# Performance work log

Measured on AMD Instinct MI355X. Metric: run time of the kernel, lower is better.

The kernel has to match this reference:

```python
import jax, jax.numpy as jnp
import numpy as np

EPS = 1e-5
C_M, C, C_Z = 256, 32, 128
N_SEQ, N_RES = 256, 1024


def setup_inputs() -> dict:
    key = jax.random.key(0)
    k1, k2, k3 = jax.random.split(key, 3)
    msa = jax.random.normal(k1, (N_SEQ, N_RES, C_M), dtype=jnp.float32)
    norm_w = jnp.ones((C_M,), dtype=jnp.float32)
    norm_b = jnp.zeros((C_M,), dtype=jnp.float32)
    w_ab = jax.random.normal(k2, (C, C_M), dtype=jnp.float32) * (1.0 / np.sqrt(C_M))
    b_ab = jnp.zeros((C,), dtype=jnp.float32)
    w_out = jax.random.normal(k3, (C_Z, C * C), dtype=jnp.float32) * (1.0 / C)
    b_out = jnp.zeros((C_Z,), dtype=jnp.float32)
    return {"msa": msa, "norm_w": norm_w, "norm_b": norm_b,
            "w_ab": w_ab, "b_ab": b_ab, "w_out": w_out, "b_out": b_out}


def reference(msa, norm_w, norm_b, w_ab, b_ab, w_out, b_out):
    # msa: (s, r, c_m) -> (r, s, c_m)
    x = jnp.transpose(msa, (1, 0, 2))
    s = x.shape[1]
    # LayerNorm over c_m
    mu = jnp.mean(x, axis=-1, keepdims=True)
    var = jnp.mean(jnp.square(x - mu), axis=-1, keepdims=True)
    xn = (x - mu) * jax.lax.rsqrt(var + EPS) * norm_w + norm_b
    # a == b: same linear applied twice to same input in the original
    a = jnp.einsum('rsm,cm->rsc', xn, w_ab) + b_ab          # (r, s, c)
    # mean over s of outer product == batched A^T A / s  -> (r, c, c)
    o = jnp.einsum('rsx,rsy->rxy', a, a) / s
    o = o.reshape(o.shape[0], C * C)                        # (r, c*c)
    pre_pair = jnp.einsum('rk,zk->rz', o, w_out) + b_out    # (r, c_z)
    r = pre_pair.shape[0]
    # unsqueeze(1).expand(r, r, c_z)
    pair = jnp.broadcast_to(pre_pair[:, None, :], (r, r, C_Z))
    return pair
```

## Files before the change

### kernel.cpp

```cpp
#include <hip/hip_runtime.h>

#define NSEQ 256
#define NRES 1024
#define CM   256
#define CC   32
#define CZ   128
#define EPS  1e-5f
#define SROW (NRES * CM)
#define MCH  16
#define XPAD 20

typedef float f4v __attribute__((ext_vector_type(4)));

__global__ void opm_setup(const float* __restrict__ nw,
                          const float* __restrict__ nb,
                          const float* __restrict__ w_ab,
                          const float* __restrict__ b_ab,
                          float* __restrict__ wt_g,
                          float* __restrict__ k12)
{
    __shared__ float wls[CM * CC];
    const int t = threadIdx.x;
    const float nwm = nw[t];
    #pragma unroll
    for (int c = 0; c < CC; ++c)
        wls[t * CC + c] = nwm * w_ab[c * CM + t];
    __syncthreads();
    for (int i = t; i < CM * CC; i += 256) wt_g[i] = wls[i];
    if (t < CC) {
        float k1 = 0.f, k2 = 0.f;
        for (int m = 0; m < CM; ++m) {
            k1 += wls[m * CC + t];
            k2 = fmaf(nb[m], w_ab[t * CM + m], k2);
        }
        k12[t]      = k1;
        k12[CC + t] = k2 + b_ab[t];
    }
}

__launch_bounds__(256, 3)
__global__ void opm_compute(const float* __restrict__ msa,
                            const float* __restrict__ wt_g,
                            const float* __restrict__ k12,
                            const float* __restrict__ w_out,
                            const float* __restrict__ b_out,
                            float* __restrict__ pre_out)
{
    __shared__ float wt[CM * CC];
    __shared__ float xt[NSEQ * XPAD];

    const int tid  = threadIdx.x;
    const int r    = blockIdx.x;
    const int wave = tid >> 6;

    const int sc4 = tid & 3;
    const int sg4 = tid >> 2;
    const int sc8 = tid & 7;
    const int sg8 = tid >> 3;
    const int c0  = sc8 << 2;

    const float* xr = msa + (size_t)r * CM;

    float4 pf[4];
    #pragma unroll
    for (int k = 0; k < 4; ++k)
        pf[k] = *(const float4*)(xr + (size_t)(sg4 + (k << 6)) * SROW + (sc4 << 2));

    #pragma unroll
    for (int k = 0; k < 8; ++k) {
        const int i = (tid + (k << 8)) << 2;
        *(float4*)&wt[i] = *(const float4*)&wt_g[i];
    }

    float G[8][4];
    #pragma unroll
    for (int j = 0; j < 8; ++j) {
        G[j][0] = 0.f; G[j][1] = 0.f; G[j][2] = 0.f; G[j][3] = 0.f;
    }
    float psum[4], pssq[4];
    #pragma unroll
    for (int k = 0; k < 4; ++k) { psum[k] = 0.f; pssq[k] = 0.f; }

    for (int mb = 0; mb < CM; mb += MCH) {
        __syncthreads();
        #pragma unroll
        for (int k = 0; k < 4; ++k) {
            *(float4*)&xt[(sg4 + (k << 6)) * XPAD + (sc4 << 2)] = pf[k];
            psum[k] += (pf[k].x + pf[k].y) + (pf[k].z + pf[k].w);
            pssq[k]  = fmaf(pf[k].x, pf[k].x, fmaf(pf[k].y, pf[k].y,
                       fmaf(pf[k].z, pf[k].z, fmaf(pf[k].w, pf[k].w, pssq[k]))));
        }
        __syncthreads();
        if (mb + MCH < CM) {
            #pragma unroll
            for (int k = 0; k < 4; ++k)
                pf[k] = *(const float4*)(xr + (size_t)(sg4 + (k << 6)) * SROW + (mb + MCH) + (sc4 << 2));
        }
        #pragma unroll
        for (int mm = 0; mm < MCH; mm += 4) {
            const float4 w0 = *(const float4*)&wt[(mb + mm + 0) * CC + c0];
            const float4 w1 = *(const float4*)&wt[(mb + mm + 1) * CC + c0];
            const float4 w2 = *(const float4*)&wt[(mb + mm + 2) * CC + c0];
            const float4 w3 = *(const float4*)&wt[(mb + mm + 3) * CC + c0];
            #pragma unroll
            for (int j = 0; j < 8; ++j) {
                const float4 x4 = *(const float4*)&xt[(sg8 + (j << 5)) * XPAD + mm];
                G[j][0] = fmaf(x4.x, w0.x, fmaf(x4.y, w1.x, fmaf(x4.z, w2.x, fmaf(x4.w, w3.x, G[j][0]))));
                G[j][1] = fmaf(x4.x, w0.y, fmaf(x4.y, w1.y, fmaf(x4.z, w2.y, fmaf(x4.w, w3.y, G[j][1]))));
                G[j][2] = fmaf(x4.x, w0.z, fmaf(x4.y, w1.z, fmaf(x4.z, w2.z, fmaf(x4.w, w3.z, G[j][2]))));
                G[j][3] = fmaf(x4.x, w0.w, fmaf(x4.y, w1.w, fmaf(x4.z, w2.w, fmaf(x4.w, w3.w, G[j][3]))));
            }
        }
    }
    __syncthreads();

    #pragma unroll
    for (int k = 0; k < 4; ++k) {
        float s1 = psum[k], s2 = pssq[k];
        s1 += __shfl_xor(s1, 1); s1 += __shfl_xor(s1, 2);
        s2 += __shfl_xor(s2, 1); s2 += __shfl_xor(s2, 2);
        if (sc4 == 0) {
            const int s = sg4 + (k << 6);
            const float mu  = s1 * (1.f / CM);
            const float var = s2 * (1.f / CM) - mu * mu;
            xt[s]        = mu;
            xt[NSEQ + s] = 1.f / sqrtf(var + EPS);
        }
    }
    __syncthreads();

    {
        const float4 k1v = *(const float4*)&k12[c0];
        const float4 k2v = *(const float4*)&k12[CC + c0];
        #pragma unroll
        for (int j = 0; j < 8; ++j) {
            const int s = sg8 + (j << 5);
            const float mu = xt[s], rstd = xt[NSEQ + s];
            float4 av;
            av.x = fmaf(rstd, G[j][0] - mu * k1v.x, k2v.x);
            av.y = fmaf(rstd, G[j][1] - mu * k1v.y, k2v.y);
            av.z = fmaf(rstd, G[j][2] - mu * k1v.z, k2v.z);
            av.w = fmaf(rstd, G[j][3] - mu * k1v.w, k2v.w);
            *(float4*)&wt[s * CC + ((sc8 ^ (s & 7)) << 2)] = av;
        }
    }
    __syncthreads();

    const int grp = wave;
    const int xs  = (tid >> 3) & 7;
    const int ys  = tid & 7;
    float4 pr0 = {0,0,0,0}, pr1 = {0,0,0,0}, pr2 = {0,0,0,0}, pr3 = {0,0,0,0};
    #pragma unroll 4
    for (int si = 0; si < 64; ++si) {
        const int s  = (grp << 6) + si;
        const int sw = si & 7;
        const float4 ax = *(const float4*)&wt[s * CC + ((xs ^ sw) << 2)];
        const float4 ay = *(const float4*)&wt[s * CC + ((ys ^ sw) << 2)];
        pr0.x = fmaf(ax.x, ay.x, pr0.x); pr0.y = fmaf(ax.x, ay.y, pr0.y);
        pr0.z = fmaf(ax.x, ay.z, pr0.z); pr0.w = fmaf(ax.x, ay.w, pr0.w);
        pr1.x = fmaf(ax.y, ay.x, pr1.x); pr1.y = fmaf(ax.y, ay.y, pr1.y);
        pr1.z = fmaf(ax.y, ay.z, pr1.z); pr1.w = fmaf(ax.y, ay.w, pr1.w);
        pr2.x = fmaf(ax.z, ay.x, pr2.x); pr2.y = fmaf(ax.z, ay.y, pr2.y);
        pr2.z = fmaf(ax.z, ay.z, pr2.z); pr2.w = fmaf(ax.z, ay.w, pr2.w);
        pr3.x = fmaf(ax.w, ay.x, pr3.x); pr3.y = fmaf(ax.w, ay.y, pr3.y);
        pr3.z = fmaf(ax.w, ay.z, pr3.z); pr3.w = fmaf(ax.w, ay.w, pr3.w);
    }
    {
        float* pb = &xt[(grp << 10) + (xs << 7) + (ys << 2)];
        *(float4*)&pb[0 << 5] = pr0;
        *(float4*)&pb[1 << 5] = pr1;
        *(float4*)&pb[2 << 5] = pr2;
        *(float4*)&pb[3 << 5] = pr3;
    }
    __syncthreads();
    {
        const float inv_s = 1.f / NSEQ;
        float4 acc = *(const float4*)&xt[(tid << 2)];
        const float4 b1 = *(const float4*)&xt[1024 + (tid << 2)];
        const float4 b2 = *(const float4*)&xt[2048 + (tid << 2)];
        const float4 b3 = *(const float4*)&xt[3072 + (tid << 2)];
        acc.x = (acc.x + b1.x + b2.x + b3.x) * inv_s;
        acc.y = (acc.y + b1.y + b2.y + b3.y) * inv_s;
        acc.z = (acc.z + b1.z + b2.z + b3.z) * inv_s;
        acc.w = (acc.w + b1.w + b2.w + b3.w) * inv_s;
        *(float4*)&xt[tid << 2] = acc;
    }
    __syncthreads();

    {
        const int z    = tid & 127;
        const int half = tid >> 7;
        const float* wrow = w_out + (size_t)z * (CC * CC) + half * 512;
        const float* op   = &xt[half * 512];
        float po = 0.f;
        #pragma unroll 8
        for (int k = 0; k < 512; k += 4) {
            const float4 o4 = *(const float4*)&op[k];
            const float4 w4 = *(const float4*)&wrow[k];
            po = fmaf(o4.x, w4.x, fmaf(o4.y, w4.y, fmaf(o4.z, w4.z, fmaf(o4.w, w4.w, po))));
        }
        xt[4096 + (half << 7) + z] = po;
    }
    __syncthreads();
    if (tid < CZ)
        pre_out[(size_t)r * CZ + tid] = xt[4096 + tid] + xt[4096 + CZ + tid] + b_out[tid];
}

__launch_bounds__(256, 8)
__global__ void opm_bcast(const float* __restrict__ pre,
                          float* __restrict__ out)
{
    const int bid = blockIdx.x;
    const int r   = bid >> 3;
    const int jb  = bid & 7;
    const int z4  = threadIdx.x & 31;
    const int jo  = threadIdx.x >> 5;

    const f4v pv = *((const f4v*)(pre + (size_t)r * CZ) + z4);
    f4v* outp = (f4v*)out + ((size_t)r * NRES + (size_t)jb * 128) * (CZ / 4);
    for (int j0 = 0; j0 < 128; j0 += 8)
        __builtin_nontemporal_store(pv, &outp[(size_t)(j0 + jo) * (CZ / 4) + z4]);
}

extern "C" void kernel_launch(void* const* d_in, const int* in_sizes, int n_in,
                              void* d_out, int out_size, void* d_ws, size_t ws_size,
                              hipStream_t stream) {
    const float* msa   = (const float*)d_in[0];
    const float* nw    = (const float*)d_in[1];
    const float* nb    = (const float*)d_in[2];
    const float* w_ab  = (const float*)d_in[3];
    const float* b_ab  = (const float*)d_in[4];
    const float* w_out = (const float*)d_in[5];
    const float* b_out = (const float*)d_in[6];
    float* out = (float*)d_out;

    float* pre  = (float*)d_ws;
    float* wt_g = pre + (size_t)NRES * CZ;
    float* k12  = wt_g + CM * CC;

    opm_setup<<<1, 256, 0, stream>>>(nw, nb, w_ab, b_ab, wt_g, k12);
    opm_compute<<<NRES, 256, 0, stream>>>(msa, wt_g, k12, w_out, b_out, pre);
    opm_bcast<<<NRES * 8, 256, 0, stream>>>(pre, out);
}
```

Before: 795.4 us.

## Process two residues per block with 8x8 register tiles sharing weight loads

```diff
diff --git a/kernel.cpp b/kernel.cpp
--- a/kernel.cpp
+++ b/kernel.cpp
@@ -9,6 +9,7 @@
 #define SROW (NRES * CM)
 #define MCH  16
 #define XPAD 20
+#define CHF  (NSEQ * XPAD)
 
 typedef float f4v __attribute__((ext_vector_type(4)));
 
@@ -38,7 +39,7 @@
     }
 }
 
-__launch_bounds__(256, 3)
+__launch_bounds__(256, 2)
 __global__ void opm_compute(const float* __restrict__ msa,
                             const float* __restrict__ wt_g,
                             const float* __restrict__ k12,
@@ -47,24 +48,22 @@
                             float* __restrict__ pre_out)
 {
     __shared__ float wt[CM * CC];
-    __shared__ float xt[NSEQ * XPAD];
-
-    const int tid  = threadIdx.x;
-    const int r    = blockIdx.x;
-    const int wave = tid >> 6;
-
-    const int sc4 = tid & 3;
-    const int sg4 = tid >> 2;
-    const int sc8 = tid & 7;
-    const int sg8 = tid >> 3;
-    const int c0  = sc8 << 2;
-
-    const float* xr = msa + (size_t)r * CM;
-
-    float4 pf[4];
-    #pragma unroll
-    for (int k = 0; k < 4; ++k)
-        pf[k] = *(const float4*)(xr + (size_t)(sg4 + (k << 6)) * SROW + (sc4 << 2));
+    __shared__ float xa[2 * CHF];
+
+    const int tid = threadIdx.x;
+    const int r0  = blockIdx.x << 1;
+    const int res = tid >> 7;
+    const int t   = tid & 127;
+
+    const int sc4 = t & 3;
+    const int sg  = t >> 2;
+    const int cg  = t & 3;
+    const int rg  = t >> 2;
+    const int c0  = cg << 3;
+
+    float* chunk = xa + res * CHF;
+    float* stat  = xa + 2 * CHF - 2048;
+    const float* xr = msa + (size_t)(r0 + res) * CM + (sc4 << 2);
 
     #pragma unroll
     for (int k = 0; k < 8; ++k) {
@@ -72,20 +71,25 @@
         *(float4*)&wt[i] = *(const float4*)&wt_g[i];
     }
 
-    float G[8][4];
-    #pragma unroll
-    for (int j = 0; j < 8; ++j) {
-        G[j][0] = 0.f; G[j][1] = 0.f; G[j][2] = 0.f; G[j][3] = 0.f;
-    }
-    float psum[4], pssq[4];
-    #pragma unroll
-    for (int k = 0; k < 4; ++k) { psum[k] = 0.f; pssq[k] = 0.f; }
+    float G[8][8];
+    #pragma unroll
+    for (int j = 0; j < 8; ++j)
+        #pragma unroll
+        for (int c = 0; c < 8; ++c) G[j][c] = 0.f;
+    float psum[8], pssq[8];
+    #pragma unroll
+    for (int k = 0; k < 8; ++k) { psum[k] = 0.f; pssq[k] = 0.f; }
+
+    float4 pf[8];
+    #pragma unroll
+    for (int k = 0; k < 8; ++k)
+        pf[k] = *(const float4*)(xr + (size_t)(sg + (k << 5)) * SROW);
 
     for (int mb = 0; mb < CM; mb += MCH) {
         __syncthreads();
         #pragma unroll
-        for (int k = 0; k < 4; ++k) {
-            *(float4*)&xt[(sg4 + (k << 6)) * XPAD + (sc4 << 2)] = pf[k];
+        for (int k = 0; k < 8; ++k) {
+            *(float4*)&chunk[(sg + (k << 5)) * XPAD + (sc4 << 2)] = pf[k];
             psum[k] += (pf[k].x + pf[k].y) + (pf[k].z + pf[k].w);
             pssq[k]  = fmaf(pf[k].x, pf[k].x, fmaf(pf[k].y, pf[k].y,
                        fmaf(pf[k].z, pf[k].z, fmaf(pf[k].w, pf[k].w, pssq[k]))));
@@ -93,69 +97,89 @@
         __syncthreads();
         if (mb + MCH < CM) {
             #pragma unroll
-            for (int k = 0; k < 4; ++k)
-                pf[k] = *(const float4*)(xr + (size_t)(sg4 + (k << 6)) * SROW + (mb + MCH) + (sc4 << 2));
+            for (int k = 0; k < 8; ++k)
+                pf[k] = *(const float4*)(xr + (size_t)(sg + (k << 5)) * SROW + (mb + MCH));
         }
         #pragma unroll
         for (int mm = 0; mm < MCH; mm += 4) {
-            const float4 w0 = *(const float4*)&wt[(mb + mm + 0) * CC + c0];
-            const float4 w1 = *(const float4*)&wt[(mb + mm + 1) * CC + c0];
-            const float4 w2 = *(const float4*)&wt[(mb + mm + 2) * CC + c0];
-            const float4 w3 = *(const float4*)&wt[(mb + mm + 3) * CC + c0];
+            float4 xv[8];
             #pragma unroll
-            for (int j = 0; j < 8; ++j) {
-                const float4 x4 = *(const float4*)&xt[(sg8 + (j << 5)) * XPAD + mm];
-                G[j][0] = fmaf(x4.x, w0.x, fmaf(x4.y, w1.x, fmaf(x4.z, w2.x, fmaf(x4.w, w3.x, G[j][0]))));
-                G[j][1] = fmaf(x4.x, w0.y, fmaf(x4.y, w1.y, fmaf(x4.z, w2.y, fmaf(x4.w, w3.y, G[j][1]))));
-                G[j][2] = fmaf(x4.x, w0.z, fmaf(x4.y, w1.z, fmaf(x4.z, w2.z, fmaf(x4.w, w3.z, G[j][2]))));
-                G[j][3] = fmaf(x4.x, w0.w, fmaf(x4.y, w1.w, fmaf(x4.z, w2.w, fmaf(x4.w, w3.w, G[j][3]))));
+            for (int j = 0; j < 8; ++j)
+                xv[j] = *(const float4*)&chunk[(rg + (j << 5)) * XPAD + mm];
+            #pragma unroll
+            for (int q = 0; q < 4; ++q) {
+                const float4 wa = *(const float4*)&wt[(mb + mm + q) * CC + c0];
+                const float4 wb = *(const float4*)&wt[(mb + mm + q) * CC + c0 + 4];
+                #pragma unroll
+                for (int j = 0; j < 8; ++j) {
+                    const float xq = (q == 0) ? xv[j].x : (q == 1) ? xv[j].y
+                                   : (q == 2) ? xv[j].z : xv[j].w;
+                    G[j][0] = fmaf(xq, wa.x, G[j][0]);
+                    G[j][1] = fmaf(xq, wa.y, G[j][1]);
+                    G[j][2] = fmaf(xq, wa.z, G[j][2]);
+                    G[j][3] = fmaf(xq, wa.w, G[j][3]);
+                    G[j][4] = fmaf(xq, wb.x, G[j][4]);
+                    G[j][5] = fmaf(xq, wb.y, G[j][5]);
+                    G[j][6] = fmaf(xq, wb.z, G[j][6]);
+                    G[j][7] = fmaf(xq, wb.w, G[j][7]);
+                }
             }
         }
     }
     __syncthreads();
 
     #pragma unroll
-    for (int k = 0; k < 4; ++k) {
+    for (int k = 0; k < 8; ++k) {
         float s1 = psum[k], s2 = pssq[k];
         s1 += __shfl_xor(s1, 1); s1 += __shfl_xor(s1, 2);
         s2 += __shfl_xor(s2, 1); s2 += __shfl_xor(s2, 2);
         if (sc4 == 0) {
-            const int s = sg4 + (k << 6);
+            const int s = sg + (k << 5);
             const float mu  = s1 * (1.f / CM);
             const float var = s2 * (1.f / CM) - mu * mu;
-            xt[s]        = mu;
-            xt[NSEQ + s] = 1.f / sqrtf(var + EPS);
-        }
-    }
-    __syncthreads();
-
+            stat[(res << 9) + s]       = mu;
+            stat[(res << 9) + 256 + s] = 1.f / sqrtf(var + EPS);
+        }
+    }
+    __syncthreads();
+
+    float* aB = res ? xa : wt;
     {
-        const float4 k1v = *(const float4*)&k12[c0];
-        const float4 k2v = *(const float4*)&k12[CC + c0];
+        const float4 k1a = *(const float4*)&k12[c0];
+        const float4 k1b = *(const float4*)&k12[c0 + 4];
+        const float4 k2a = *(const float4*)&k12[CC + c0];
+        const float4 k2b = *(const float4*)&k12[CC + c0 + 4];
         #pragma unroll
         for (int j = 0; j < 8; ++j) {
-            const int s = sg8 + (j << 5);
-            const float mu = xt[s], rstd = xt[NSEQ + s];
-            float4 av;
-            av.x = fmaf(rstd, G[j][0] - mu * k1v.x, k2v.x);
-            av.y = fmaf(rstd, G[j][1] - mu * k1v.y, k2v.y);
-            av.z = fmaf(rstd, G[j][2] - mu * k1v.z, k2v.z);
-            av.w = fmaf(rstd, G[j][3] - mu * k1v.w, k2v.w);
-            *(float4*)&wt[s * CC + ((sc8 ^ (s & 7)) << 2)] = av;
-        }
-    }
-    __syncthreads();
-
-    const int grp = wave;
-    const int xs  = (tid >> 3) & 7;
-    const int ys  = tid & 7;
+            const int s = rg + (j << 5);
+            const float mu   = stat[(res << 9) + s];
+            const float rstd = stat[(res << 9) + 256 + s];
+            float4 va, vb;
+            va.x = fmaf(rstd, G[j][0] - mu * k1a.x, k2a.x);
+            va.y = fmaf(rstd, G[j][1] - mu * k1a.y, k2a.y);
+            va.z = fmaf(rstd, G[j][2] - mu * k1a.z, k2a.z);
+            va.w = fmaf(rstd, G[j][3] - mu * k1a.w, k2a.w);
+            vb.x = fmaf(rstd, G[j][4] - mu * k1b.x, k2b.x);
+            vb.y = fmaf(rstd, G[j][5] - mu * k1b.y, k2b.y);
+            vb.z = fmaf(rstd, G[j][6] - mu * k1b.z, k2b.z);
+            vb.w = fmaf(rstd, G[j][7] - mu * k1b.w, k2b.w);
+            const int sw = s & 7;
+            *(float4*)&aB[s * CC + ((((cg << 1)    ) ^ sw) << 2)] = va;
+            *(float4*)&aB[s * CC + ((((cg << 1) | 1) ^ sw) << 2)] = vb;
+        }
+    }
+    __syncthreads();
+
+    const int h  = (t >> 6) & 1;
+    const int xs = (t >> 3) & 7;
+    const int ys = t & 7;
     float4 pr0 = {0,0,0,0}, pr1 = {0,0,0,0}, pr2 = {0,0,0,0}, pr3 = {0,0,0,0};
     #pragma unroll 4
-    for (int si = 0; si < 64; ++si) {
-        const int s  = (grp << 6) + si;
-        const int sw = si & 7;
-        const float4 ax = *(const float4*)&wt[s * CC + ((xs ^ sw) << 2)];
-        const float4 ay = *(const float4*)&wt[s * CC + ((ys ^ sw) << 2)];
+    for (int si = 0; si < 128; ++si) {
+        const int s  = (h << 7) + si;
+        const int sw = s & 7;
+        const float4 ax = *(const float4*)&aB[s * CC + ((xs ^ sw) << 2)];
+        const float4 ay = *(const float4*)&aB[s * CC + ((ys ^ sw) << 2)];
         pr0.x = fmaf(ax.x, ay.x, pr0.x); pr0.y = fmaf(ax.x, ay.y, pr0.y);
         pr0.z = fmaf(ax.x, ay.z, pr0.z); pr0.w = fmaf(ax.x, ay.w, pr0.w);
         pr1.x = fmaf(ax.y, ay.x, pr1.x); pr1.y = fmaf(ax.y, ay.y, pr1.y);
@@ -165,45 +189,48 @@
         pr3.x = fmaf(ax.w, ay.x, pr3.x); pr3.y = fmaf(ax.w, ay.y, pr3.y);
         pr3.z = fmaf(ax.w, ay.z, pr3.z); pr3.w = fmaf(ax.w, ay.w, pr3.w);
     }
+    float* pb = &stat[(res << 10) + ((xs << 2) * CC) + (ys << 2)];
+    if (h) {
+        *(float4*)&pb[0 * CC] = pr0;
+        *(float4*)&pb[1 * CC] = pr1;
+        *(float4*)&pb[2 * CC] = pr2;
+        *(float4*)&pb[3 * CC] = pr3;
+    }
+    __syncthreads();
+    if (!h) {
+        const float inv_s = 1.f / NSEQ;
+        float4 q0 = *(const float4*)&pb[0 * CC];
+        float4 q1 = *(const float4*)&pb[1 * CC];
+        float4 q2 = *(const float4*)&pb[2 * CC];
+        float4 q3 = *(const float4*)&pb[3 * CC];
+        q0.x = (q0.x + pr0.x) * inv_s; q0.y = (q0.y + pr0.y) * inv_s;
+        q0.z = (q0.z + pr0.z) * inv_s; q0.w = (q0.w + pr0.w) * inv_s;
+        q1.x = (q1.x + pr1.x) * inv_s; q1.y = (q1.y + pr1.y) * inv_s;
+        q1.z = (q1.z + pr1.z) * inv_s; q1.w = (q1.w + pr1.w) * inv_s;
+        q2.x = (q2.x + pr2.x) * inv_s; q2.y = (q2.y + pr2.y) * inv_s;
+        q2.z = (q2.z + pr2.z) * inv_s; q2.w = (q2.w + pr2.w) * inv_s;
+        q3.x = (q3.x + pr3.x) * inv_s; q3.y = (q3.y + pr3.y) * inv_s;
+        q3.z = (q3.z + pr3.z) * inv_s; q3.w = (q3.w + pr3.w) * inv_s;
+        *(float4*)&pb[0 * CC] = q0;
+        *(float4*)&pb[1 * CC] = q1;
+        *(float4*)&pb[2 * CC] = q2;
+        *(float4*)&pb[3 * CC] = q3;
+    }
+    __syncthreads();
+
     {
-        float* pb = &xt[(grp << 10) + (xs << 7) + (ys << 2)];
-        *(float4*)&pb[0 << 5] = pr0;
-        *(float4*)&pb[1 << 5] = pr1;
-        *(float4*)&pb[2 << 5] = pr2;
-        *(float4*)&pb[3 << 5] = pr3;
-    }
-    __syncthreads();
-    {
-        const float inv_s = 1.f / NSEQ;
-        float4 acc = *(const float4*)&xt[(tid << 2)];
-        const float4 b1 = *(const float4*)&xt[1024 + (tid << 2)];
-        const float4 b2 = *(const float4*)&xt[2048 + (tid << 2)];
-        const float4 b3 = *(const float4*)&xt[3072 + (tid << 2)];
-        acc.x = (acc.x + b1.x + b2.x + b3.x) * inv_s;
-        acc.y = (acc.y + b1.y + b2.y + b3.y) * inv_s;
-        acc.z = (acc.z + b1.z + b2.z + b3.z) * inv_s;
-        acc.w = (acc.w + b1.w + b2.w + b3.w) * inv_s;
-        *(float4*)&xt[tid << 2] = acc;
-    }
-    __syncthreads();
-
-    {
-        const int z    = tid & 127;
-        const int half = tid >> 7;
-        const float* wrow = w_out + (size_t)z * (CC * CC) + half * 512;
-        const float* op   = &xt[half * 512];
+        const int z = t;
+        const float* wrow = w_out + (size_t)z * (CC * CC);
+        const float* op   = &stat[res << 10];
         float po = 0.f;
         #pragma unroll 8
-        for (int k = 0; k < 512; k += 4) {
+        for (int k = 0; k < CC * CC; k += 4) {
             const float4 o4 = *(const float4*)&op[k];
             const float4 w4 = *(const float4*)&wrow[k];
             po = fmaf(o4.x, w4.x, fmaf(o4.y, w4.y, fmaf(o4.z, w4.z, fmaf(o4.w, w4.w, po))));
         }
-        xt[4096 + (half << 7) + z] = po;
-    }
-    __syncthreads();
-    if (tid < CZ)
-        pre_out[(size_t)r * CZ + tid] = xt[4096 + tid] + xt[4096 + CZ + tid] + b_out[tid];
+        pre_out[(size_t)(r0 + res) * CZ + z] = po + b_out[z];
+    }
 }
 
 __launch_bounds__(256, 8)
@@ -239,6 +266,6 @@
     float* k12  = wt_g + CM * CC;
 
     opm_setup<<<1, 256, 0, stream>>>(nw, nb, w_ab, b_ab, wt_g, k12);
-    opm_compute<<<NRES, 256, 0, stream>>>(msa, wt_g, k12, w_out, b_out, pre);
+    opm_compute<<<NRES / 2, 256, 0, stream>>>(msa, wt_g, k12, w_out, b_out, pre);
     opm_bcast<<<NRES * 8, 256, 0, stream>>>(pre, out);
 }
```

Result: slower. 826.4 us (+3.9%).

## Split fused kernel into contiguous LayerNorm-projection pass and per-residue outer-product pass

Applied to the files above, without the earlier changes.

```diff
diff --git a/kernel.cpp b/kernel.cpp
--- a/kernel.cpp
+++ b/kernel.cpp
@@ -6,7 +6,6 @@
 #define CC   32
 #define CZ   128
 #define EPS  1e-5f
-#define SROW (NRES * CM)
 #define MCH  16
 #define XPAD 20
 
@@ -39,19 +38,17 @@
 }
 
 __launch_bounds__(256, 3)
-__global__ void opm_compute(const float* __restrict__ msa,
-                            const float* __restrict__ wt_g,
-                            const float* __restrict__ k12,
-                            const float* __restrict__ w_out,
-                            const float* __restrict__ b_out,
-                            float* __restrict__ pre_out)
+__global__ void opm_lnproj(const float* __restrict__ msa,
+                           const float* __restrict__ wt_g,
+                           const float* __restrict__ k12,
+                           float* __restrict__ a_ws)
 {
     __shared__ float wt[CM * CC];
-    __shared__ float xt[NSEQ * XPAD];
-
-    const int tid  = threadIdx.x;
-    const int r    = blockIdx.x;
-    const int wave = tid >> 6;
+    __shared__ float xs[256 * XPAD];
+
+    const int tid = threadIdx.x;
+    const int s   = blockIdx.x >> 2;
+    const int r0  = (blockIdx.x & 3) << 8;
 
     const int sc4 = tid & 3;
     const int sg4 = tid >> 2;
@@ -59,12 +56,7 @@
     const int sg8 = tid >> 3;
     const int c0  = sc8 << 2;
 
-    const float* xr = msa + (size_t)r * CM;
-
-    float4 pf[4];
-    #pragma unroll
-    for (int k = 0; k < 4; ++k)
-        pf[k] = *(const float4*)(xr + (size_t)(sg4 + (k << 6)) * SROW + (sc4 << 2));
+    const float* xr = msa + ((size_t)s * NRES + r0) * CM + (sc4 << 2);
 
     #pragma unroll
     for (int k = 0; k < 8; ++k) {
@@ -81,11 +73,16 @@
     #pragma unroll
     for (int k = 0; k < 4; ++k) { psum[k] = 0.f; pssq[k] = 0.f; }
 
+    float4 pf[4];
+    #pragma unroll
+    for (int k = 0; k < 4; ++k)
+        pf[k] = *(const float4*)(xr + (size_t)(sg4 + (k << 6)) * CM);
+
     for (int mb = 0; mb < CM; mb += MCH) {
         __syncthreads();
         #pragma unroll
         for (int k = 0; k < 4; ++k) {
-            *(float4*)&xt[(sg4 + (k << 6)) * XPAD + (sc4 << 2)] = pf[k];
+            *(float4*)&xs[(sg4 + (k << 6)) * XPAD + (sc4 << 2)] = pf[k];
             psum[k] += (pf[k].x + pf[k].y) + (pf[k].z + pf[k].w);
             pssq[k]  = fmaf(pf[k].x, pf[k].x, fmaf(pf[k].y, pf[k].y,
                        fmaf(pf[k].z, pf[k].z, fmaf(pf[k].w, pf[k].w, pssq[k]))));
@@ -94,7 +91,7 @@
         if (mb + MCH < CM) {
             #pragma unroll
             for (int k = 0; k < 4; ++k)
-                pf[k] = *(const float4*)(xr + (size_t)(sg4 + (k << 6)) * SROW + (mb + MCH) + (sc4 << 2));
+                pf[k] = *(const float4*)(xr + (size_t)(sg4 + (k << 6)) * CM + (mb + MCH));
         }
         #pragma unroll
         for (int mm = 0; mm < MCH; mm += 4) {
@@ -104,7 +101,7 @@
             const float4 w3 = *(const float4*)&wt[(mb + mm + 3) * CC + c0];
             #pragma unroll
             for (int j = 0; j < 8; ++j) {
-                const float4 x4 = *(const float4*)&xt[(sg8 + (j << 5)) * XPAD + mm];
+                const float4 x4 = *(const float4*)&xs[(sg8 + (j << 5)) * XPAD + mm];
                 G[j][0] = fmaf(x4.x, w0.x, fmaf(x4.y, w1.x, fmaf(x4.z, w2.x, fmaf(x4.w, w3.x, G[j][0]))));
                 G[j][1] = fmaf(x4.x, w0.y, fmaf(x4.y, w1.y, fmaf(x4.z, w2.y, fmaf(x4.w, w3.y, G[j][1]))));
                 G[j][2] = fmaf(x4.x, w0.z, fmaf(x4.y, w1.z, fmaf(x4.z, w2.z, fmaf(x4.w, w3.z, G[j][2]))));
@@ -120,11 +117,11 @@
         s1 += __shfl_xor(s1, 1); s1 += __shfl_xor(s1, 2);
         s2 += __shfl_xor(s2, 1); s2 += __shfl_xor(s2, 2);
         if (sc4 == 0) {
-            const int s = sg4 + (k << 6);
+            const int row = sg4 + (k << 6);
             const float mu  = s1 * (1.f / CM);
             const float var = s2 * (1.f / CM) - mu * mu;
-            xt[s]        = mu;
-            xt[NSEQ + s] = 1.f / sqrtf(var + EPS);
+            xs[row]       = mu;
+            xs[256 + row] = 1.f / sqrtf(var + EPS);
         }
     }
     __syncthreads();
@@ -132,30 +129,56 @@
     {
         const float4 k1v = *(const float4*)&k12[c0];
         const float4 k2v = *(const float4*)&k12[CC + c0];
+        float* ab = a_ws + ((size_t)s * NRES + r0) * CC + c0;
         #pragma unroll
         for (int j = 0; j < 8; ++j) {
-            const int s = sg8 + (j << 5);
-            const float mu = xt[s], rstd = xt[NSEQ + s];
+            const int row = sg8 + (j << 5);
+            const float mu = xs[row], rstd = xs[256 + row];
             float4 av;
             av.x = fmaf(rstd, G[j][0] - mu * k1v.x, k2v.x);
             av.y = fmaf(rstd, G[j][1] - mu * k1v.y, k2v.y);
             av.z = fmaf(rstd, G[j][2] - mu * k1v.z, k2v.z);
             av.w = fmaf(rstd, G[j][3] - mu * k1v.w, k2v.w);
-            *(float4*)&wt[s * CC + ((sc8 ^ (s & 7)) << 2)] = av;
+            *(float4*)&ab[(size_t)row * CC] = av;
+        }
+    }
+}
+
+__launch_bounds__(256, 3)
+__global__ void opm_outer(const float* __restrict__ a_ws,
+                          const float* __restrict__ w_out,
+                          const float* __restrict__ b_out,
+                          float* __restrict__ pre_out)
+{
+    __shared__ float axs[NSEQ * CC];
+    __shared__ float sc[4096 + 256];
+
+    const int tid  = threadIdx.x;
+    const int r    = blockIdx.x;
+    const int wave = tid >> 6;
+
+    {
+        const int slot = tid & 7;
+        const int s8   = tid >> 3;
+        #pragma unroll
+        for (int k = 0; k < 8; ++k) {
+            const int s_ = s8 + (k << 5);
+            const float4 v = *(const float4*)&a_ws[((size_t)s_ * NRES + r) * CC + (slot << 2)];
+            *(float4*)&axs[s_ * CC + ((slot ^ (s_ & 7)) << 2)] = v;
         }
     }
     __syncthreads();
 
     const int grp = wave;
-    const int xs  = (tid >> 3) & 7;
-    const int ys  = tid & 7;
+    const int xs_ = (tid >> 3) & 7;
+    const int ys_ = tid & 7;
     float4 pr0 = {0,0,0,0}, pr1 = {0,0,0,0}, pr2 = {0,0,0,0}, pr3 = {0,0,0,0};
     #pragma unroll 4
     for (int si = 0; si < 64; ++si) {
-        const int s  = (grp << 6) + si;
-        const int sw = si & 7;
-        const float4 ax = *(const float4*)&wt[s * CC + ((xs ^ sw) << 2)];
-        const float4 ay = *(const float4*)&wt[s * CC + ((ys ^ sw) << 2)];
+        const int s_ = (grp << 6) + si;
+        const int sw = s_ & 7;
+        const float4 ax = *(const float4*)&axs[s_ * CC + ((xs_ ^ sw) << 2)];
+        const float4 ay = *(const float4*)&axs[s_ * CC + ((ys_ ^ sw) << 2)];
         pr0.x = fmaf(ax.x, ay.x, pr0.x); pr0.y = fmaf(ax.x, ay.y, pr0.y);
         pr0.z = fmaf(ax.x, ay.z, pr0.z); pr0.w = fmaf(ax.x, ay.w, pr0.w);
         pr1.x = fmaf(ax.y, ay.x, pr1.x); pr1.y = fmaf(ax.y, ay.y, pr1.y);
@@ -166,24 +189,24 @@
         pr3.z = fmaf(ax.w, ay.z, pr3.z); pr3.w = fmaf(ax.w, ay.w, pr3.w);
     }
     {
-        float* pb = &xt[(grp << 10) + (xs << 7) + (ys << 2)];
-        *(float4*)&pb[0 << 5] = pr0;
-        *(float4*)&pb[1 << 5] = pr1;
-        *(float4*)&pb[2 << 5] = pr2;
-        *(float4*)&pb[3 << 5] = pr3;
+        float* pb = &sc[(grp << 10) + ((xs_ << 2) * CC) + (ys_ << 2)];
+        *(float4*)&pb[0 * CC] = pr0;
+        *(float4*)&pb[1 * CC] = pr1;
+        *(float4*)&pb[2 * CC] = pr2;
+        *(float4*)&pb[3 * CC] = pr3;
     }
     __syncthreads();
     {
         const float inv_s = 1.f / NSEQ;
-        float4 acc = *(const float4*)&xt[(tid << 2)];
-        const float4 b1 = *(const float4*)&xt[1024 + (tid << 2)];
-        const float4 b2 = *(const float4*)&xt[2048 + (tid << 2)];
-        const float4 b3 = *(const float4*)&xt[3072 + (tid << 2)];
+        float4 acc = *(const float4*)&sc[(tid << 2)];
+        const float4 b1 = *(const float4*)&sc[1024 + (tid << 2)];
+        const float4 b2 = *(const float4*)&sc[2048 + (tid << 2)];
+        const float4 b3 = *(const float4*)&sc[3072 + (tid << 2)];
         acc.x = (acc.x + b1.x + b2.x + b3.x) * inv_s;
         acc.y = (acc.y + b1.y + b2.y + b3.y) * inv_s;
         acc.z = (acc.z + b1.z + b2.z + b3.z) * inv_s;
         acc.w = (acc.w + b1.w + b2.w + b3.w) * inv_s;
-        *(float4*)&xt[tid << 2] = acc;
+        *(float4*)&sc[tid << 2] = acc;
     }
     __syncthreads();
 
@@ -191,7 +214,7 @@
         const int z    = tid & 127;
         const int half = tid >> 7;
         const float* wrow = w_out + (size_t)z * (CC * CC) + half * 512;
-        const float* op   = &xt[half * 512];
+        const float* op   = &sc[half * 512];
         float po = 0.f;
         #pragma unroll 8
         for (int k = 0; k < 512; k += 4) {
@@ -199,11 +222,12 @@
             const float4 w4 = *(const float4*)&wrow[k];
             po = fmaf(o4.x, w4.x, fmaf(o4.y, w4.y, fmaf(o4.z, w4.z, fmaf(o4.w, w4.w, po))));
         }
-        xt[4096 + (half << 7) + z] = po;
+        sc[4096 + (half << 7) + (z & 127)] = po;
+        if (half) sc[4096 + 128 + z] = po;
     }
     __syncthreads();
     if (tid < CZ)
-        pre_out[(size_t)r * CZ + tid] = xt[4096 + tid] + xt[4096 + CZ + tid] + b_out[tid];
+        pre_out[(size_t)r * CZ + tid] = sc[4096 + tid] + sc[4096 + CZ + tid] + b_out[tid];
 }
 
 __launch_bounds__(256, 8)
@@ -237,8 +261,10 @@
     float* pre  = (float*)d_ws;
     float* wt_g = pre + (size_t)NRES * CZ;
     float* k12  = wt_g + CM * CC;
+    float* a_ws = k12 + 64;
 
     opm_setup<<<1, 256, 0, stream>>>(nw, nb, w_ab, b_ab, wt_g, k12);
-    opm_compute<<<NRES, 256, 0, stream>>>(msa, wt_g, k12, w_out, b_out, pre);
+    opm_lnproj<<<NRES, 256, 0, stream>>>(msa, wt_g, k12, a_ws);
+    opm_outer<<<NRES, 256, 0, stream>>>(a_ws, w_out, b_out, pre);
     opm_bcast<<<NRES * 8, 256, 0, stream>>>(pre, out);
 }
```

Measured after the change: 825.2 us. +3.7%, slower.
